# Optimization experiments

Measured on AMD Instinct MI355X. Metric: run time of the kernel, lower is better.

The kernel has to match this reference:

```python
import jax, jax.numpy as jnp
import numpy as np

N_NODES = 50000
N_EDGES = 800000
IN_CH = 128
HID = 128


def _linear_params(key, fan_in, fan_out):
    kw, kb = jax.random.split(key)
    bound = 1.0 / np.sqrt(fan_in)
    W = jax.random.uniform(kw, (fan_in, fan_out), jnp.float32, -bound, bound)
    b = jax.random.uniform(kb, (fan_out,), jnp.float32, -bound, bound)
    return W, b


def setup_inputs() -> dict:
    key = jax.random.key(0)
    ks = jax.random.split(key, 11)
    x = jax.random.normal(ks[0], (N_NODES, IN_CH), jnp.float32)
    guidance_features = jax.random.normal(ks[1], (N_NODES, HID), jnp.float32)
    edge_index = jax.random.randint(ks[2], (2, N_EDGES), 0, N_NODES, jnp.int64)
    node_W, node_b = _linear_params(ks[3], IN_CH, HID)
    nbr_W, nbr_b = _linear_params(ks[4], IN_CH, HID)
    gud_W, gud_b = _linear_params(ks[5], HID, HID)
    enc_W, enc_b = _linear_params(ks[6], 3 * HID, HID)
    vp_W1, vp_b1 = _linear_params(ks[7], HID, HID // 2)
    vp_W2, vp_b2 = _linear_params(ks[8], HID // 2, 1)
    pol_W1, pol_b1 = _linear_params(ks[9], HID, HID)
    pol_W2, pol_b2 = _linear_params(ks[10], HID, 1)
    return dict(x=x, edge_index=edge_index, guidance_features=guidance_features,
                node_W=node_W, node_b=node_b, nbr_W=nbr_W, nbr_b=nbr_b,
                gud_W=gud_W, gud_b=gud_b, enc_W=enc_W, enc_b=enc_b,
                vp_W1=vp_W1, vp_b1=vp_b1, vp_W2=vp_W2, vp_b2=vp_b2,
                pol_W1=pol_W1, pol_b1=pol_b1, pol_W2=pol_W2, pol_b2=pol_b2)


def reference(x, edge_index, guidance_features,
              node_W, node_b, nbr_W, nbr_b, gud_W, gud_b,
              enc_W, enc_b, vp_W1, vp_b1, vp_W2, vp_b2,
              pol_W1, pol_b1, pol_W2, pol_b2):
    row, col = edge_index[0], edge_index[1]
    # Edge-wise gathers feeding three linear transforms -> [E, 3*HID] state
    node_feat = x[row] @ node_W + node_b            # [E, HID]
    nbr_feat = x[col] @ nbr_W + nbr_b               # [E, HID]
    gud_feat = guidance_features[col] @ gud_W + gud_b  # [E, HID]
    state = jnp.concatenate([node_feat, nbr_feat, gud_feat], axis=1)
    # state_encoder (eval mode: dropout = identity)
    enc = jax.nn.relu(state @ enc_W + enc_b)        # [E, HID]
    # value_predictor
    value_preds = jax.nn.relu(enc @ vp_W1 + vp_b1) @ vp_W2 + vp_b2  # [E, 1]
    # policy_net
    action_probs = jax.nn.sigmoid(
        jax.nn.relu(enc @ pol_W1 + pol_b1) @ pol_W2 + pol_b2)      # [E, 1]
    actions = (action_probs > 0.5).astype(x.dtype)  # eval-mode actions
    value_loss = jnp.zeros((), x.dtype)             # eval mode, labels=None
    return value_preds, action_probs, actions, value_loss
```

## Files before the change

kernel.cpp:

```cpp
#include <hip/hip_runtime.h>
#include <math.h>

#define N_NODES 50000
#define N_EDGES 800000

typedef __attribute__((ext_vector_type(8))) short short8_t;
typedef __attribute__((ext_vector_type(4))) float float4_t;

union U8 { short8_t v; unsigned short u[8]; };

__device__ __forceinline__ unsigned short bf16_rn(float f) {
    unsigned u = __float_as_uint(f);
    u += 0x7fffu + ((u >> 16) & 1u);
    return (unsigned short)(u >> 16);
}
__device__ __forceinline__ float bf2f(unsigned short h) {
    return __uint_as_float((unsigned)h << 16);
}
__device__ __forceinline__ void split3(float f, unsigned short& s0,
                                       unsigned short& s1, unsigned short& s2) {
    s0 = bf16_rn(f);  float r = f - bf2f(s0);
    s1 = bf16_rn(r);  r -= bf2f(s1);
    s2 = bf16_rn(r);
}
__device__ __forceinline__ void split3t(float f, unsigned short& s0,
                                        unsigned short& s1, unsigned short& s2) {
    unsigned u = __float_as_uint(f);
    s0 = (unsigned short)(u >> 16);
    float r = f - bf2f(s0);
    unsigned v = __float_as_uint(r);
    s1 = (unsigned short)(v >> 16);
    float r2 = r - bf2f(s1);
    s2 = bf16_rn(r2);
}


__global__ __launch_bounds__(256) void prep_kernel(
    const float* __restrict__ node_W, const float* __restrict__ node_b,
    const float* __restrict__ nbr_W,  const float* __restrict__ nbr_b,
    const float* __restrict__ gud_W,  const float* __restrict__ gud_b,
    const float* __restrict__ enc_W,  const float* __restrict__ enc_b,
    const float* __restrict__ vp_W1,  const float* __restrict__ vp_b1,
    const float* __restrict__ vp_W2,  const float* __restrict__ pol_W1,
    const float* __restrict__ pol_b1, const float* __restrict__ pol_W2,
    unsigned short* __restrict__ BTn0, unsigned short* __restrict__ BTn1,
    unsigned short* __restrict__ BTn2,
    unsigned short* __restrict__ BTg0, unsigned short* __restrict__ BTg1,
    unsigned short* __restrict__ BTg2,
    unsigned short* __restrict__ BTw0, unsigned short* __restrict__ BTw1,
    unsigned short* __restrict__ BTw2,
    float* __restrict__ cb, float* __restrict__ b1c, float* __restrict__ W2c,
    int* __restrict__ flags)
{
    const int k = blockIdx.x;
    const int j = threadIdx.x;
    if (j < 128) {
        float a = 0.f, b = 0.f;
        #pragma unroll 4
        for (int m = 0; m < 128; ++m) {
            a = fmaf(node_W[k * 128 + m], enc_W[m * 128 + j], a);
            b = fmaf(gud_W [k * 128 + m], enc_W[(256 + m) * 128 + j], b);
        }
        size_t i1 = (size_t)j * 128 + k;
        split3(a, BTn0[i1], BTn1[i1], BTn2[i1]);
        split3(b, BTg0[i1], BTg1[i1], BTg2[i1]);
    } else {
        const int n = j - 128;
        float a = 0.f;
        #pragma unroll 4
        for (int m = 0; m < 128; ++m)
            a = fmaf(nbr_W[k * 128 + m], enc_W[(128 + m) * 128 + n], a);
        size_t i2 = (size_t)(128 + n) * 128 + k;
        split3(a, BTn0[i2], BTn1[i2], BTn2[i2]);
    }
    if (j < 192) {
        float wv = (j < 64) ? vp_W1[k * 64 + j] : pol_W1[k * 128 + (j - 64)];
        size_t iw = (size_t)j * 128 + k;
        split3(wv, BTw0[iw], BTw1[iw], BTw2[iw]);
    }
    if (k == 0) {
        if (j < 128) {
            float cc = enc_b[j];
            for (int m = 0; m < 128; ++m) {
                cc = fmaf(node_b[m], enc_W[m * 128 + j], cc);
                cc = fmaf(nbr_b [m], enc_W[(128 + m) * 128 + j], cc);
                cc = fmaf(gud_b [m], enc_W[(256 + m) * 128 + j], cc);
            }
            cb[j] = cc;
        }
        if (j < 192) {
            b1c[j] = (j < 64) ? vp_b1[j] : pol_b1[j - 64];
            W2c[j] = (j < 64) ? vp_W2[j] : pol_W2[j - 64];
        }
        if (j < 64) {
            const int l = j, li = l & 15, lq = l >> 4;
            U8 A, B;
            #pragma unroll
            for (int u = 0; u < 8; ++u) { A.u[u] = 0; B.u[u] = 0; }
            if (lq == 0) {
                A.u[0] = bf16_rn((float)(li + 1));
                A.u[1] = bf16_rn(1.0f);
                B.u[0] = bf16_rn(1.0f);
                B.u[1] = bf16_rn((float)(100 * (li + 1)));
            }
            float4_t d = (float4_t){0.f, 0.f, 0.f, 0.f};
            d = __builtin_amdgcn_mfma_f32_16x16x32_bf16(A.v, B.v, d, 0, 0, 0);
            if (l == 17) {
                flags[0] = (fabsf(d[2] - 702.f) < 1.0f) ? 1 : 0;
            }
        }
    }
}

__global__ __launch_bounds__(256, 3) void node_kernel(
    const float* __restrict__ x, const float* __restrict__ g,
    const unsigned short* __restrict__ BTn0, const unsigned short* __restrict__ BTn1,
    const unsigned short* __restrict__ BTn2,
    const unsigned short* __restrict__ BTg0, const unsigned short* __restrict__ BTg1,
    const unsigned short* __restrict__ BTg2,
    const float* __restrict__ cb, const int* __restrict__ flags,
    float* __restrict__ P, float* __restrict__ Q)
{
    __shared__ unsigned short a0s[4 * 64 * 8];
    __shared__ unsigned short a1s[4 * 64 * 8];
    __shared__ unsigned short a2s[4 * 64 * 8];
    const int t = threadIdx.x;
    const int w = t >> 6, lane = t & 63;
    const int i16 = lane & 15, q = lane >> 4;
    const int base = blockIdx.x * 64;
    const int swap = flags[0];
    const int el = t >> 2, hh = t & 3;
    int nodeL = base + el; if (nodeL > N_NODES - 1) nodeL = N_NODES - 1;
    const float* xrow = x + (size_t)nodeL * 128 + hh * 8;
    const float* grow = g + (size_t)nodeL * 128 + hh * 8;

    float4_t acc[4][4];
    #pragma unroll
    for (int mt = 0; mt < 4; ++mt)
        #pragma unroll
        for (int nt = 0; nt < 4; ++nt) acc[mt][nt] = (float4_t){0.f, 0.f, 0.f, 0.f};

    float4 pv0 = *(const float4*)(xrow);
    float4 pv1 = *(const float4*)(xrow + 4);

    for (int kc = 0; kc < 8; ++kc) {
        U8 s0, s1, s2;
        {
            float e[8] = {pv0.x, pv0.y, pv0.z, pv0.w, pv1.x, pv1.y, pv1.z, pv1.w};
            #pragma unroll
            for (int u = 0; u < 8; ++u) split3t(e[u], s0.u[u], s1.u[u], s2.u[u]);
        }
        __syncthreads();
        {
            size_t off = ((size_t)hh * 64 + el) * 8;
            *(short8_t*)(a0s + off) = s0.v;
            *(short8_t*)(a1s + off) = s1.v;
            *(short8_t*)(a2s + off) = s2.v;
        }
        __syncthreads();
        if (kc < 7) {
            const float* nsrc = (kc + 1 < 4) ? (xrow + (kc + 1) * 32)
                                             : (grow + (kc + 1 - 4) * 32);
            pv0 = *(const float4*)(nsrc);
            pv1 = *(const float4*)(nsrc + 4);
        }
        if (kc < 4) {
            short8_t b0[4], b1v[4], b2v[4];
            #pragma unroll
            for (int ntl = 0; ntl < 4; ++ntl) {
                int ntg = w + ntl * 4;
                size_t roff = ((size_t)(ntg * 16 + i16)) * 128 + kc * 32 + q * 8;
                b0[ntl]  = *(const short8_t*)(BTn0 + roff);
                b1v[ntl] = *(const short8_t*)(BTn1 + roff);
                b2v[ntl] = *(const short8_t*)(BTn2 + roff);
            }
            #pragma unroll
            for (int mt = 0; mt < 4; ++mt) {
                size_t aoff = ((size_t)q * 64 + mt * 16 + i16) * 8;
                short8_t a0 = *(const short8_t*)(a0s + aoff);
                short8_t a1 = *(const short8_t*)(a1s + aoff);
                short8_t a2 = *(const short8_t*)(a2s + aoff);
                #pragma unroll
                for (int ntl = 0; ntl < 4; ++ntl) {
                    float4_t c = acc[mt][ntl];
                    c = __builtin_amdgcn_mfma_f32_16x16x32_bf16(a0, b0[ntl],  c, 0, 0, 0);
                    c = __builtin_amdgcn_mfma_f32_16x16x32_bf16(a0, b1v[ntl], c, 0, 0, 0);
                    c = __builtin_amdgcn_mfma_f32_16x16x32_bf16(a1, b0[ntl],  c, 0, 0, 0);
                    c = __builtin_amdgcn_mfma_f32_16x16x32_bf16(a0, b2v[ntl], c, 0, 0, 0);
                    c = __builtin_amdgcn_mfma_f32_16x16x32_bf16(a1, b1v[ntl], c, 0, 0, 0);
                    c = __builtin_amdgcn_mfma_f32_16x16x32_bf16(a2, b0[ntl],  c, 0, 0, 0);
                    acc[mt][ntl] = c;
                }
            }
        } else {
            short8_t b0[2], b1v[2], b2v[2];
            #pragma unroll
            for (int ntl = 0; ntl < 2; ++ntl) {
                int ntg = w + (ntl + 2) * 4;
                size_t roff = ((size_t)((ntg - 8) * 16 + i16)) * 128 + (kc - 4) * 32 + q * 8;
                b0[ntl]  = *(const short8_t*)(BTg0 + roff);
                b1v[ntl] = *(const short8_t*)(BTg1 + roff);
                b2v[ntl] = *(const short8_t*)(BTg2 + roff);
            }
            #pragma unroll
            for (int mt = 0; mt < 4; ++mt) {
                size_t aoff = ((size_t)q * 64 + mt * 16 + i16) * 8;
                short8_t a0 = *(const short8_t*)(a0s + aoff);
                short8_t a1 = *(const short8_t*)(a1s + aoff);
                short8_t a2 = *(const short8_t*)(a2s + aoff);
                #pragma unroll
                for (int ntl = 0; ntl < 2; ++ntl) {
                    float4_t c = acc[mt][ntl + 2];
                    c = __builtin_amdgcn_mfma_f32_16x16x32_bf16(a0, b0[ntl],  c, 0, 0, 0);
                    c = __builtin_amdgcn_mfma_f32_16x16x32_bf16(a0, b1v[ntl], c, 0, 0, 0);
                    c = __builtin_amdgcn_mfma_f32_16x16x32_bf16(a1, b0[ntl],  c, 0, 0, 0);
                    c = __builtin_amdgcn_mfma_f32_16x16x32_bf16(a0, b2v[ntl], c, 0, 0, 0);
                    c = __builtin_amdgcn_mfma_f32_16x16x32_bf16(a1, b1v[ntl], c, 0, 0, 0);
                    c = __builtin_amdgcn_mfma_f32_16x16x32_bf16(a2, b0[ntl],  c, 0, 0, 0);
                    acc[mt][ntl + 2] = c;
                }
            }
        }
    }

    if (!swap) {
        #pragma unroll
        for (int mt = 0; mt < 4; ++mt)
            #pragma unroll
            for (int ntl = 0; ntl < 4; ++ntl) {
                int ntg = w + ntl * 4;
                int chan = ntg * 16 + i16;
                bool isP = (ntg < 8);
                float bias = isP ? cb[chan] : 0.f;
                #pragma unroll
                for (int r = 0; r < 4; ++r) {
                    int node = base + mt * 16 + q * 4 + r;
                    if (node < N_NODES) {
                        if (isP) P[(size_t)node * 128 + chan] = acc[mt][ntl][r] + bias;
                        else     Q[(size_t)node * 128 + (chan - 128)] = acc[mt][ntl][r];
                    }
                }
            }
    } else {
        #pragma unroll
        for (int mt = 0; mt < 4; ++mt) {
            int node = base + mt * 16 + i16;
            if (node < N_NODES) {
                #pragma unroll
                for (int ntl = 0; ntl < 4; ++ntl) {
                    int ntg = w + ntl * 4;
                    int chanb = ntg * 16 + q * 4;
                    bool isP = (ntg < 8);
                    float4 vv;
                    vv.x = acc[mt][ntl][0] + (isP ? cb[chanb + 0] : 0.f);
                    vv.y = acc[mt][ntl][1] + (isP ? cb[chanb + 1] : 0.f);
                    vv.z = acc[mt][ntl][2] + (isP ? cb[chanb + 2] : 0.f);
                    vv.w = acc[mt][ntl][3] + (isP ? cb[chanb + 3] : 0.f);
                    if (isP) *(float4*)(P + (size_t)node * 128 + chanb) = vv;
                    else     *(float4*)(Q + (size_t)node * 128 + chanb - 128) = vv;
                }
            }
        }
    }
}

__global__ __launch_bounds__(256, 3) void edge_kernel(
    const int* __restrict__ ei,
    const float* __restrict__ P, const float* __restrict__ Q,
    const unsigned short* __restrict__ BTw0, const unsigned short* __restrict__ BTw1,
    const unsigned short* __restrict__ BTw2,
    const float* __restrict__ b1c, const float* __restrict__ W2c,
    const float* __restrict__ vp_b2, const float* __restrict__ pol_b2,
    const int* __restrict__ flags,
    float* __restrict__ out)
{
    __shared__ unsigned short enc0[4 * 128 * 8];
    __shared__ unsigned short enc1[4 * 128 * 8];
    __shared__ unsigned short enc2[4 * 128 * 8];
    __shared__ float vpart[512], ppart[512];

    const int t = threadIdx.x;
    const int w = t >> 6, lane = t & 63;
    const int i16 = lane & 15, q = lane >> 4;
    const int e0 = blockIdx.x * 128;
    const int ntg0 = w * 3;
    const int el = t >> 1, hh = t & 1;
    const int swap = flags[0];

    const int rowI = ei[e0 + el];
    const int colI = ei[N_EDGES + e0 + el];
    const float* Pp = P + (size_t)rowI * 128 + hh * 16;
    const float* Qp = Q + (size_t)colI * 128 + hh * 16;

    float4_t acc[8][3];
    #pragma unroll
    for (int mt = 0; mt < 8; ++mt)
        #pragma unroll
        for (int nt = 0; nt < 3; ++nt) acc[mt][nt] = (float4_t){0.f, 0.f, 0.f, 0.f};

    float4 pv[4], qv[4];
    #pragma unroll
    for (int i = 0; i < 4; ++i) {
        pv[i] = *(const float4*)(Pp + i * 4);
        qv[i] = *(const float4*)(Qp + i * 4);
    }

    for (int kc = 0; kc < 4; ++kc) {
        U8 g0[2], g1[2], g2[2];
        #pragma unroll
        for (int i = 0; i < 4; ++i) {
            float ev[4] = {fmaxf(pv[i].x + qv[i].x, 0.f), fmaxf(pv[i].y + qv[i].y, 0.f),
                           fmaxf(pv[i].z + qv[i].z, 0.f), fmaxf(pv[i].w + qv[i].w, 0.f)};
            #pragma unroll
            for (int u = 0; u < 4; ++u) {
                int idx = i * 4 + u;
                split3t(ev[u], g0[idx >> 3].u[idx & 7], g1[idx >> 3].u[idx & 7],
                        g2[idx >> 3].u[idx & 7]);
            }
        }
        __syncthreads();
        #pragma unroll
        for (int hb = 0; hb < 2; ++hb) {
            size_t off = ((size_t)(2 * hh + hb) * 128 + el) * 8;
            *(short8_t*)(enc0 + off) = g0[hb].v;
            *(short8_t*)(enc1 + off) = g1[hb].v;
            *(short8_t*)(enc2 + off) = g2[hb].v;
        }
        __syncthreads();
        if (kc < 3) {
            #pragma unroll
            for (int i = 0; i < 4; ++i) {
                pv[i] = *(const float4*)(Pp + (kc + 1) * 32 + i * 4);
                qv[i] = *(const float4*)(Qp + (kc + 1) * 32 + i * 4);
            }
        }
        short8_t b0[3], b1f[3], b2f[3];
        #pragma unroll
        for (int ntl = 0; ntl < 3; ++ntl) {
            size_t roff = ((size_t)((ntg0 + ntl) * 16 + i16)) * 128 + kc * 32 + q * 8;
            b0[ntl]  = *(const short8_t*)(BTw0 + roff);
            b1f[ntl] = *(const short8_t*)(BTw1 + roff);
            b2f[ntl] = *(const short8_t*)(BTw2 + roff);
        }
        #pragma unroll
        for (int mt = 0; mt < 8; ++mt) {
            size_t aoff = ((size_t)q * 128 + mt * 16 + i16) * 8;
            short8_t a0 = *(const short8_t*)(enc0 + aoff);
            short8_t a1 = *(const short8_t*)(enc1 + aoff);
            short8_t a2 = *(const short8_t*)(enc2 + aoff);
            #pragma unroll
            for (int ntl = 0; ntl < 3; ++ntl) {
                float4_t c = acc[mt][ntl];
                c = __builtin_amdgcn_mfma_f32_16x16x32_bf16(a0, b0[ntl],  c, 0, 0, 0);
                c = __builtin_amdgcn_mfma_f32_16x16x32_bf16(a0, b1f[ntl], c, 0, 0, 0);
                c = __builtin_amdgcn_mfma_f32_16x16x32_bf16(a1, b0[ntl],  c, 0, 0, 0);
                c = __builtin_amdgcn_mfma_f32_16x16x32_bf16(a0, b2f[ntl], c, 0, 0, 0);
                c = __builtin_amdgcn_mfma_f32_16x16x32_bf16(a1, b1f[ntl], c, 0, 0, 0);
                c = __builtin_amdgcn_mfma_f32_16x16x32_bf16(a2, b0[ntl],  c, 0, 0, 0);
                acc[mt][ntl] = c;
            }
        }
    }

    if (!swap) {
        #pragma unroll
        for (int mt = 0; mt < 8; ++mt) {
            float vs[4] = {0.f, 0.f, 0.f, 0.f}, ps[4] = {0.f, 0.f, 0.f, 0.f};
            #pragma unroll
            for (int ntl = 0; ntl < 3; ++ntl) {
                int ntg = ntg0 + ntl;
                int n = ntg * 16 + i16;
                float b1s = b1c[n], w2s = W2c[n];
                bool isv = (ntg < 4);
                #pragma unroll
                for (int r = 0; r < 4; ++r) {
                    float hv = fmaxf(acc[mt][ntl][r] + b1s, 0.f) * w2s;
                    if (isv) vs[r] += hv; else ps[r] += hv;
                }
            }
            #pragma unroll
            for (int off = 1; off < 16; off <<= 1)
                #pragma unroll
                for (int r = 0; r < 4; ++r) {
                    vs[r] += __shfl_xor(vs[r], off, 64);
                    ps[r] += __shfl_xor(ps[r], off, 64);
                }
            if (i16 == 0)
                #pragma unroll
                for (int r = 0; r < 4; ++r) {
                    int eidx = mt * 16 + q * 4 + r;
                    vpart[w * 128 + eidx] = vs[r];
                    ppart[w * 128 + eidx] = ps[r];
                }
        }
    } else {
        #pragma unroll
        for (int mt = 0; mt < 8; ++mt) {
            float v = 0.f, p = 0.f;
            #pragma unroll
            for (int ntl = 0; ntl < 3; ++ntl) {
                int ntg = ntg0 + ntl;
                bool isv = (ntg < 4);
                #pragma unroll
                for (int r = 0; r < 4; ++r) {
                    int n = ntg * 16 + q * 4 + r;
                    float hv = fmaxf(acc[mt][ntl][r] + b1c[n], 0.f) * W2c[n];
                    if (isv) v += hv; else p += hv;
                }
            }
            v += __shfl_xor(v, 16, 64); v += __shfl_xor(v, 32, 64);
            p += __shfl_xor(p, 16, 64); p += __shfl_xor(p, 32, 64);
            if (q == 0) {
                int eidx = mt * 16 + i16;
                vpart[w * 128 + eidx] = v;
                ppart[w * 128 + eidx] = p;
            }
        }
    }
    __syncthreads();
    if (t < 128) {
        float v  = vpart[t] + vpart[128 + t] + vpart[256 + t] + vpart[384 + t] + vp_b2[0];
        float pl = ppart[t] + ppart[128 + t] + ppart[256 + t] + ppart[384 + t] + pol_b2[0];
        float prob = 1.0f / (1.0f + expf(-pl));
        int e = e0 + t;
        out[e] = v;
        out[N_EDGES + e] = prob;
        out[2 * N_EDGES + e] = (prob > 0.5f) ? 1.0f : 0.0f;
    }
    if (blockIdx.x == 0 && t == 0) out[3 * N_EDGES] = 0.0f;
}

extern "C" void kernel_launch(void* const* d_in, const int* in_sizes, int n_in,
                              void* d_out, int out_size, void* d_ws, size_t ws_size,
                              hipStream_t stream) {
    const float* x      = (const float*)d_in[0];
    const int*   ei     = (const int*)  d_in[1];
    const float* gf     = (const float*)d_in[2];
    const float* node_W = (const float*)d_in[3];
    const float* node_b = (const float*)d_in[4];
    const float* nbr_W  = (const float*)d_in[5];
    const float* nbr_b  = (const float*)d_in[6];
    const float* gud_W  = (const float*)d_in[7];
    const float* gud_b  = (const float*)d_in[8];
    const float* enc_W  = (const float*)d_in[9];
    const float* enc_b  = (const float*)d_in[10];
    const float* vp_W1  = (const float*)d_in[11];
    const float* vp_b1  = (const float*)d_in[12];
    const float* vp_W2  = (const float*)d_in[13];
    const float* vp_b2  = (const float*)d_in[14];
    const float* pol_W1 = (const float*)d_in[15];
    const float* pol_b1 = (const float*)d_in[16];
    const float* pol_W2 = (const float*)d_in[17];
    const float* pol_b2 = (const float*)d_in[18];
    float* out = (float*)d_out;

    unsigned char* wsb = (unsigned char*)d_ws;
    unsigned short* BTn0 = (unsigned short*)(wsb + 0);
    unsigned short* BTn1 = (unsigned short*)(wsb + 65536);
    unsigned short* BTn2 = (unsigned short*)(wsb + 131072);
    unsigned short* BTg0 = (unsigned short*)(wsb + 196608);
    unsigned short* BTg1 = (unsigned short*)(wsb + 229376);
    unsigned short* BTg2 = (unsigned short*)(wsb + 262144);
    unsigned short* BTw0 = (unsigned short*)(wsb + 294912);
    unsigned short* BTw1 = (unsigned short*)(wsb + 344064);
    unsigned short* BTw2 = (unsigned short*)(wsb + 393216);
    float* cb   = (float*)(wsb + 442368);
    float* b1c  = (float*)(wsb + 442880);
    float* W2c  = (float*)(wsb + 443648);
    int*   flags= (int*)  (wsb + 444416);
    float* Pd   = (float*)(wsb + 444480);
    float* Qd   = Pd + (size_t)N_NODES * 128;

    prep_kernel<<<dim3(128), dim3(256), 0, stream>>>(
        node_W, node_b, nbr_W, nbr_b, gud_W, gud_b, enc_W, enc_b,
        vp_W1, vp_b1, vp_W2, pol_W1, pol_b1, pol_W2,
        BTn0, BTn1, BTn2, BTg0, BTg1, BTg2, BTw0, BTw1, BTw2,
        cb, b1c, W2c, flags);

    node_kernel<<<dim3((N_NODES + 63) / 64), dim3(256), 0, stream>>>(
        x, gf, BTn0, BTn1, BTn2, BTg0, BTg1, BTg2, cb, flags, Pd, Qd);

    edge_kernel<<<dim3(N_EDGES / 128), dim3(256), 0, stream>>>(
        ei, Pd, Qd, BTw0, BTw1, BTw2, b1c, W2c, vp_b2, pol_b2, flags, out);
}
```

Measured before the change: 557.1 us.

## Shrink edge tile to 64 and stage full K in LDS once

The edge kernel now handles 64 edges per block instead of 128. Each thread gathers its whole 32-channel slice of P and Q up front and writes all four K-chunks of the split-bf16 activations to shared memory, so only one barrier is needed instead of two per chunk. The accumulator array is halved, which reduces register pressure, and the grid doubles. The cost is that weight fragments are reloaded for every 64 edges rather than every 128, and the in-loop prefetch of the next gather chunk is dropped, so gather latency is no longer overlapped with the MFMA work.

```diff
diff --git a/kernel.cpp b/kernel.cpp
--- a/kernel.cpp
+++ b/kernel.cpp
@@ -274,89 +274,78 @@
     const int* __restrict__ flags,
     float* __restrict__ out)
 {
-    __shared__ unsigned short enc0[4 * 128 * 8];
-    __shared__ unsigned short enc1[4 * 128 * 8];
-    __shared__ unsigned short enc2[4 * 128 * 8];
-    __shared__ float vpart[512], ppart[512];
+    __shared__ unsigned short enc0[16 * 64 * 8];
+    __shared__ unsigned short enc1[16 * 64 * 8];
+    __shared__ unsigned short enc2[16 * 64 * 8];
+    __shared__ float vpart[256], ppart[256];
 
     const int t = threadIdx.x;
     const int w = t >> 6, lane = t & 63;
     const int i16 = lane & 15, q = lane >> 4;
-    const int e0 = blockIdx.x * 128;
+    const int e0 = blockIdx.x * 64;
     const int ntg0 = w * 3;
-    const int el = t >> 1, hh = t & 1;
+    const int el = t >> 2, hh = t & 3;
     const int swap = flags[0];
 
     const int rowI = ei[e0 + el];
     const int colI = ei[N_EDGES + e0 + el];
-    const float* Pp = P + (size_t)rowI * 128 + hh * 16;
-    const float* Qp = Q + (size_t)colI * 128 + hh * 16;
-
-    float4_t acc[8][3];
+    const float* Pp = P + (size_t)rowI * 128 + hh * 32;
+    const float* Qp = Q + (size_t)colI * 128 + hh * 32;
+
+    {
+        float4 pv[8], qv[8];
+        #pragma unroll
+        for (int i = 0; i < 8; ++i) {
+            pv[i] = *(const float4*)(Pp + i * 4);
+            qv[i] = *(const float4*)(Qp + i * 4);
+        }
+        #pragma unroll
+        for (int j = 0; j < 4; ++j) {
+            float4 pa = pv[2 * j], pb = pv[2 * j + 1];
+            float4 qa = qv[2 * j], qb = qv[2 * j + 1];
+            float ev[8] = {
+                fmaxf(pa.x + qa.x, 0.f), fmaxf(pa.y + qa.y, 0.f),
+                fmaxf(pa.z + qa.z, 0.f), fmaxf(pa.w + qa.w, 0.f),
+                fmaxf(pb.x + qb.x, 0.f), fmaxf(pb.y + qb.y, 0.f),
+                fmaxf(pb.z + qb.z, 0.f), fmaxf(pb.w + qb.w, 0.f)};
+            U8 s0, s1, s2;
+            #pragma unroll
+            for (int u = 0; u < 8; ++u) split3t(ev[u], s0.u[u], s1.u[u], s2.u[u]);
+            size_t off = ((size_t)(hh * 4 + j) * 64 + el) * 8;
+            *(short8_t*)(enc0 + off) = s0.v;
+            *(short8_t*)(enc1 + off) = s1.v;
+            *(short8_t*)(enc2 + off) = s2.v;
+        }
+    }
+    __syncthreads();
+
+    float4_t acc[4][3];
     #pragma unroll
-    for (int mt = 0; mt < 8; ++mt)
+    for (int mt = 0; mt < 4; ++mt)
         #pragma unroll
         for (int nt = 0; nt < 3; ++nt) acc[mt][nt] = (float4_t){0.f, 0.f, 0.f, 0.f};
 
-    float4 pv[4], qv[4];
     #pragma unroll
-    for (int i = 0; i < 4; ++i) {
-        pv[i] = *(const float4*)(Pp + i * 4);
-        qv[i] = *(const float4*)(Qp + i * 4);
-    }
-
     for (int kc = 0; kc < 4; ++kc) {
-        U8 g0[2], g1[2], g2[2];
-        #pragma unroll
-        for (int i = 0; i < 4; ++i) {
-            float ev[4] = {fmaxf(pv[i].x + qv[i].x, 0.f), fmaxf(pv[i].y + qv[i].y, 0.f),
-                           fmaxf(pv[i].z + qv[i].z, 0.f), fmaxf(pv[i].w + qv[i].w, 0.f)};
-            #pragma unroll
-            for (int u = 0; u < 4; ++u) {
-                int idx = i * 4 + u;
-                split3t(ev[u], g0[idx >> 3].u[idx & 7], g1[idx >> 3].u[idx & 7],
-                        g2[idx >> 3].u[idx & 7]);
-            }
-        }
-        __syncthreads();
-        #pragma unroll
-        for (int hb = 0; hb < 2; ++hb) {
-            size_t off = ((size_t)(2 * hh + hb) * 128 + el) * 8;
-            *(short8_t*)(enc0 + off) = g0[hb].v;
-            *(short8_t*)(enc1 + off) = g1[hb].v;
-            *(short8_t*)(enc2 + off) = g2[hb].v;
-        }
-        __syncthreads();
-        if (kc < 3) {
-            #pragma unroll
-            for (int i = 0; i < 4; ++i) {
-                pv[i] = *(const float4*)(Pp + (kc + 1) * 32 + i * 4);
-                qv[i] = *(const float4*)(Qp + (kc + 1) * 32 + i * 4);
-            }
-        }
-        short8_t b0[3], b1f[3], b2f[3];
         #pragma unroll
         for (int ntl = 0; ntl < 3; ++ntl) {
             size_t roff = ((size_t)((ntg0 + ntl) * 16 + i16)) * 128 + kc * 32 + q * 8;
-            b0[ntl]  = *(const short8_t*)(BTw0 + roff);
-            b1f[ntl] = *(const short8_t*)(BTw1 + roff);
-            b2f[ntl] = *(const short8_t*)(BTw2 + roff);
-        }
-        #pragma unroll
-        for (int mt = 0; mt < 8; ++mt) {
-            size_t aoff = ((size_t)q * 128 + mt * 16 + i16) * 8;
-            short8_t a0 = *(const short8_t*)(enc0 + aoff);
-            short8_t a1 = *(const short8_t*)(enc1 + aoff);
-            short8_t a2 = *(const short8_t*)(enc2 + aoff);
-            #pragma unroll
-            for (int ntl = 0; ntl < 3; ++ntl) {
+            short8_t b0 = *(const short8_t*)(BTw0 + roff);
+            short8_t b1 = *(const short8_t*)(BTw1 + roff);
+            short8_t b2 = *(const short8_t*)(BTw2 + roff);
+            #pragma unroll
+            for (int mt = 0; mt < 4; ++mt) {
+                size_t aoff = ((size_t)(kc * 4 + q) * 64 + mt * 16 + i16) * 8;
+                short8_t a0 = *(const short8_t*)(enc0 + aoff);
+                short8_t a1 = *(const short8_t*)(enc1 + aoff);
+                short8_t a2 = *(const short8_t*)(enc2 + aoff);
                 float4_t c = acc[mt][ntl];
-                c = __builtin_amdgcn_mfma_f32_16x16x32_bf16(a0, b0[ntl],  c, 0, 0, 0);
-                c = __builtin_amdgcn_mfma_f32_16x16x32_bf16(a0, b1f[ntl], c, 0, 0, 0);
-                c = __builtin_amdgcn_mfma_f32_16x16x32_bf16(a1, b0[ntl],  c, 0, 0, 0);
-                c = __builtin_amdgcn_mfma_f32_16x16x32_bf16(a0, b2f[ntl], c, 0, 0, 0);
-                c = __builtin_amdgcn_mfma_f32_16x16x32_bf16(a1, b1f[ntl], c, 0, 0, 0);
-                c = __builtin_amdgcn_mfma_f32_16x16x32_bf16(a2, b0[ntl],  c, 0, 0, 0);
+                c = __builtin_amdgcn_mfma_f32_16x16x32_bf16(a0, b0, c, 0, 0, 0);
+                c = __builtin_amdgcn_mfma_f32_16x16x32_bf16(a0, b1, c, 0, 0, 0);
+                c = __builtin_amdgcn_mfma_f32_16x16x32_bf16(a1, b0, c, 0, 0, 0);
+                c = __builtin_amdgcn_mfma_f32_16x16x32_bf16(a0, b2, c, 0, 0, 0);
+                c = __builtin_amdgcn_mfma_f32_16x16x32_bf16(a1, b1, c, 0, 0, 0);
+                c = __builtin_amdgcn_mfma_f32_16x16x32_bf16(a2, b0, c, 0, 0, 0);
                 acc[mt][ntl] = c;
             }
         }
@@ -364,7 +353,7 @@
 
     if (!swap) {
         #pragma unroll
-        for (int mt = 0; mt < 8; ++mt) {
+        for (int mt = 0; mt < 4; ++mt) {
             float vs[4] = {0.f, 0.f, 0.f, 0.f}, ps[4] = {0.f, 0.f, 0.f, 0.f};
             #pragma unroll
             for (int ntl = 0; ntl < 3; ++ntl) {
@@ -389,13 +378,13 @@
                 #pragma unroll
                 for (int r = 0; r < 4; ++r) {
                     int eidx = mt * 16 + q * 4 + r;
-                    vpart[w * 128 + eidx] = vs[r];
-                    ppart[w * 128 + eidx] = ps[r];
+                    vpart[w * 64 + eidx] = vs[r];
+                    ppart[w * 64 + eidx] = ps[r];
                 }
         }
     } else {
         #pragma unroll
-        for (int mt = 0; mt < 8; ++mt) {
+        for (int mt = 0; mt < 4; ++mt) {
             float v = 0.f, p = 0.f;
             #pragma unroll
             for (int ntl = 0; ntl < 3; ++ntl) {
@@ -412,15 +401,15 @@
             p += __shfl_xor(p, 16, 64); p += __shfl_xor(p, 32, 64);
             if (q == 0) {
                 int eidx = mt * 16 + i16;
-                vpart[w * 128 + eidx] = v;
-                ppart[w * 128 + eidx] = p;
+                vpart[w * 64 + eidx] = v;
+                ppart[w * 64 + eidx] = p;
             }
         }
     }
     __syncthreads();
-    if (t < 128) {
-        float v  = vpart[t] + vpart[128 + t] + vpart[256 + t] + vpart[384 + t] + vp_b2[0];
-        float pl = ppart[t] + ppart[128 + t] + ppart[256 + t] + ppart[384 + t] + pol_b2[0];
+    if (t < 64) {
+        float v  = vpart[t] + vpart[64 + t] + vpart[128 + t] + vpart[192 + t] + vp_b2[0];
+        float pl = ppart[t] + ppart[64 + t] + ppart[128 + t] + ppart[192 + t] + pol_b2[0];
         float prob = 1.0f / (1.0f + expf(-pl));
         int e = e0 + t;
         out[e] = v;
@@ -480,6 +469,6 @@
     node_kernel<<<dim3((N_NODES + 63) / 64), dim3(256), 0, stream>>>(
         x, gf, BTn0, BTn1, BTn2, BTg0, BTg1, BTg2, cb, flags, Pd, Qd);
 
-    edge_kernel<<<dim3(N_EDGES / 128), dim3(256), 0, stream>>>(
+    edge_kernel<<<dim3(N_EDGES / 64), dim3(256), 0, stream>>>(
         ei, Pd, Qd, BTw0, BTw1, BTw2, b1c, W2c, vp_b2, pol_b2, flags, out);
 }
```

New measurement: 575.0 us. 3.2% more time.
